# Kernel optimization log

Hardware: AMD Instinct MI355X
Metric: run time of the kernel (lower is better)

The kernel has to match this reference:

```python
import jax, jax.numpy as jnp
import numpy as np

VOCAB, EMBED, HIDDEN, FEAT = 193, 256, 512, 512
MAX_LEN = 15


def setup_inputs() -> dict:
    key = jax.random.key(0)
    ks = jax.random.split(key, 12)
    B = 8192
    s = 0.05  # small init scale for weights
    return {
        "img_feats": jax.random.normal(ks[0], (B, FEAT), jnp.float32),
        "text": jax.random.randint(ks[1], (B, MAX_LEN), 0, VOCAB, jnp.int64),
        "emb": jax.random.uniform(ks[2], (VOCAB, EMBED), jnp.float32, -0.1, 0.1),
        "W_proj": jax.random.normal(ks[3], (HIDDEN, FEAT), jnp.float32) * s,
        "b_proj": jnp.zeros((HIDDEN,), jnp.float32),
        "W_ih": jax.random.normal(ks[4], (3 * HIDDEN, EMBED), jnp.float32) * s,
        "W_hh": jax.random.normal(ks[5], (3 * HIDDEN, HIDDEN), jnp.float32) * s,
        "b_ih": jax.random.normal(ks[6], (3 * HIDDEN,), jnp.float32) * s,
        "b_hh": jax.random.normal(ks[7], (3 * HIDDEN,), jnp.float32) * s,
        "W_out": jax.random.uniform(ks[8], (VOCAB, HIDDEN), jnp.float32, -0.1, 0.1),
        "b_out": jnp.zeros((VOCAB,), jnp.float32),
    }


def reference(img_feats, text, emb, W_proj, b_proj, W_ih, W_hh, b_ih, b_hh, W_out, b_out):
    # h0 = project(img_feats)   [B, H]
    h0 = img_feats @ W_proj.T + b_proj
    # Teacher-forced decoder inputs: tokens text[:, 0..13] -> embeddings [T=14, B, E]
    xs = emb[text[:, : MAX_LEN - 1]].transpose(1, 0, 2)

    def gru_step(h, x):
        gi = x @ W_ih.T + b_ih   # [B, 3H]
        gh = h @ W_hh.T + b_hh   # [B, 3H]
        i_r, i_z, i_n = jnp.split(gi, 3, axis=-1)
        h_r, h_z, h_n = jnp.split(gh, 3, axis=-1)
        r = jax.nn.sigmoid(i_r + h_r)
        z = jax.nn.sigmoid(i_z + h_z)
        n = jnp.tanh(i_n + r * h_n)
        h_new = (1.0 - z) * n + z * h
        return h_new, h_new

    _, hs = jax.lax.scan(gru_step, h0, xs)  # hs: [T, B, H]
    preds = hs @ W_out.T + b_out            # [T, B, V]
    return preds.transpose(1, 0, 2)         # [B, T=14, V]
```

## Files before the change

kernel.cpp:

```cpp
#include <hip/hip_runtime.h>
#include <stdint.h>

using bf16x8 = __attribute__((ext_vector_type(8))) __bf16;
using f32x4  = __attribute__((ext_vector_type(4))) float;

#define AS1 __attribute__((address_space(1)))
#define AS3 __attribute__((address_space(3)))

constexpr size_t OFF_WHH   = 0;
constexpr size_t OFF_WPROJ = OFF_WHH   + (size_t)1536*512*2;
constexpr size_t OFF_WOUT  = OFF_WPROJ + (size_t)512*512*2;
constexpr size_t OFF_BHN   = OFF_WOUT  + (size_t)256*512*2;
constexpr size_t OFF_BPROJ = OFF_BHN   + 512*4;
constexpr size_t OFF_BOUT  = OFF_BPROJ + 512*4;
constexpr size_t OFF_EP    = OFF_BOUT  + 256*4;
constexpr size_t OFF_HS    = OFF_EP    + (size_t)193*1536*4;
constexpr size_t OFF_IMG   = OFF_HS    + (size_t)15*8192*512*2;
constexpr size_t WS_NEED   = OFF_IMG   + (size_t)8192*512*2;

__device__ __forceinline__ short f2bf(float f) {
  union { float f; unsigned u; } v; v.f = f;
  unsigned u = v.u;
  u += 0x7FFFu + ((u >> 16) & 1u);
  return (short)(u >> 16);
}
__device__ __forceinline__ float bf2f(short s) {
  union { float f; unsigned u; } v; v.u = ((unsigned)(unsigned short)s) << 16;
  return v.f;
}
__device__ __forceinline__ float sigm(float x) { return 1.f / (1.f + __expf(-x)); }
__device__ __forceinline__ float tanh_fast(float x) {
  x = fminf(fmaxf(x, -15.f), 15.f);
  float e = __expf(-2.f * x);
  return (1.f - e) / (1.f + e);
}

template<int ROWS, int WAVES>
__device__ __forceinline__ void stage_tile(const short* __restrict__ src, size_t row0,
                                           int stride, int k0, char* lds, int tid) {
  const int w = tid >> 6;
  const int lane = tid & 63;
#pragma unroll
  for (int s = 0; s < ROWS / (8 * WAVES); ++s) {
    const int rowbase = s * (8 * WAVES) + w * 8;
    const int row = rowbase + (lane >> 3);
    const int colE = ((lane & 7) ^ (row & 7)) * 8;
    const short* g = src + (row0 + (size_t)row) * (size_t)stride + k0 + colE;
    __builtin_amdgcn_global_load_lds((const AS1 int*)g, (AS3 int*)(lds + rowbase * 128),
                                     16, 0, 0);
  }
}

__device__ __forceinline__ bf16x8 read_frag(const char* lds, int row, int ks, int lane) {
  const int kb = ks * 64 + ((lane >> 4) << 4);
  return *(const bf16x8*)(lds + row * 128 + (kb ^ ((row & 7) << 4)));
}

__global__ void prep_kernel(const float* __restrict__ W_proj, const float* __restrict__ b_proj,
                            const float* __restrict__ W_hh, const float* __restrict__ b_hh,
                            const float* __restrict__ W_out, const float* __restrict__ b_out,
                            short* __restrict__ whh, short* __restrict__ wproj,
                            short* __restrict__ wout,
                            float* __restrict__ bhn, float* __restrict__ bproj,
                            float* __restrict__ bout) {
  const int total = 1536*512 + 512*512 + 256*512 + 512 + 512 + 256;
  const int stride = gridDim.x * blockDim.x;
  for (int i = blockIdx.x * blockDim.x + threadIdx.x; i < total; i += stride) {
    int j = i;
    if (j < 1536*512) { whh[j] = f2bf(W_hh[j]); continue; }
    j -= 1536*512;
    if (j < 512*512) { wproj[j] = f2bf(W_proj[j]); continue; }
    j -= 512*512;
    if (j < 256*512) {
      int r = j / 512, c = j % 512;
      wout[j] = f2bf(r < 193 ? W_out[r*512 + c] : 0.f);
      continue;
    }
    j -= 256*512;
    if (j < 512) { bhn[j] = b_hh[1024 + j]; continue; }
    j -= 512;
    if (j < 512) { bproj[j] = b_proj[j]; continue; }
    j -= 512;
    bout[j] = (j < 193) ? b_out[j] : 0.f;
  }
}

__global__ void embproj_kernel(const float* __restrict__ emb, const float* __restrict__ W_ih,
                               const float* __restrict__ b_ih, const float* __restrict__ b_hh,
                               float* __restrict__ ep) {
  const int idx = blockIdx.x * blockDim.x + threadIdx.x;
  if (idx >= 193 * 1536) return;
  const int v = idx / 1536, c = idx % 1536;
  const float* er = emb + (size_t)v * 256;
  const float* wr = W_ih + (size_t)c * 256;
  float s = 0.f;
#pragma unroll 4
  for (int k = 0; k < 256; k += 4) {
    const float4 a = *(const float4*)(er + k);
    const float4 b = *(const float4*)(wr + k);
    s += a.x * b.x + a.y * b.y + a.z * b.z + a.w * b.w;
  }
  s += b_ih[c] + (c < 1024 ? b_hh[c] : 0.f);
  ep[idx] = s;
}

__global__ void imgcvt_kernel(const float* __restrict__ img, short* __restrict__ imgbf) {
  const int i = blockIdx.x * blockDim.x + threadIdx.x;
  const float4 v = *(const float4*)(img + (size_t)i * 4);
  short4 o; o.x = f2bf(v.x); o.y = f2bf(v.y); o.z = f2bf(v.z); o.w = f2bf(v.w);
  *(short4*)(imgbf + (size_t)i * 4) = o;
}

template<int MODE>
__global__ __launch_bounds__(512, 1)
void gemm_kernel(const short* __restrict__ A, const short* __restrict__ Bw,
                 const float* __restrict__ bias, float* __restrict__ out_f,
                 short* __restrict__ out_bf) {
  __shared__ __align__(16) char smem[49152];
  char* ldsA = smem;
  char* ldsB = smem + 16384;
  const int tid = threadIdx.x;
  const int lane = tid & 63;
  const int w = tid >> 6;
  const int wr = w >> 2, wc = w & 3;
  const unsigned m0 = blockIdx.x * 128;
  const int j0 = blockIdx.y * 256;

  f32x4 acc[4][4];
#pragma unroll
  for (int a = 0; a < 4; ++a)
#pragma unroll
    for (int b = 0; b < 4; ++b) acc[a][b] = f32x4{0.f, 0.f, 0.f, 0.f};

  for (int it = 0; it < 8; ++it) {
    const int k0 = it * 64;
    __syncthreads();
    if (MODE == 0) {
      stage_tile<128, 8>(A, m0, 512, k0, ldsA, tid);
    } else {
#pragma unroll
      for (int s = 0; s < 2; ++s) {
        const int rowbase = s * 64 + w * 8;
        const int row = rowbase + (lane >> 3);
        const unsigned m = m0 + row;
        const unsigned b = m / 14u, t = m - b * 14u;
        const int colE = ((lane & 7) ^ (row & 7)) * 8;
        const short* g = A + ((size_t)t * 8192 + b) * 512 + k0 + colE;
        __builtin_amdgcn_global_load_lds((const AS1 int*)g, (AS3 int*)(ldsA + rowbase * 128),
                                         16, 0, 0);
      }
    }
    stage_tile<256, 8>(Bw, (size_t)j0, 512, k0, ldsB, tid);
    __syncthreads();
#pragma unroll
    for (int ks = 0; ks < 2; ++ks) {
      bf16x8 af[4];
#pragma unroll
      for (int mi = 0; mi < 4; ++mi)
        af[mi] = read_frag(ldsA, wr*64 + mi*16 + (lane & 15), ks, lane);
#pragma unroll
      for (int ji = 0; ji < 4; ++ji) {
        bf16x8 bfm = read_frag(ldsB, wc*64 + ji*16 + (lane & 15), ks, lane);
#pragma unroll
        for (int mi = 0; mi < 4; ++mi)
          acc[mi][ji] = __builtin_amdgcn_mfma_f32_16x16x32_bf16(af[mi], bfm, acc[mi][ji], 0, 0, 0);
      }
    }
  }
#pragma unroll
  for (int ji = 0; ji < 4; ++ji) {
    const int j = j0 + wc*64 + ji*16 + (lane & 15);
    const float bj = bias[j];
#pragma unroll
    for (int mi = 0; mi < 4; ++mi) {
#pragma unroll
      for (int i = 0; i < 4; ++i) {
        const size_t m = m0 + wr*64 + mi*16 + ((lane >> 4) * 4) + i;
        const float v = acc[mi][ji][i] + bj;
        if (MODE == 0) {
          out_bf[m * 512 + j] = f2bf(v);
        } else {
          if (j < 193) out_f[m * 193 + j] = v;
        }
      }
    }
  }
}

__global__ __launch_bounds__(256, 2)
void gate_kernel(const short* __restrict__ Hbf, const short* __restrict__ whh,
                 const int* __restrict__ text, const int t,
                 const float* __restrict__ embproj, const float* __restrict__ bhn,
                 short* __restrict__ hs_out) {
  __shared__ __align__(16) char smem[40960];
  char* ldsA = smem;
  char* ldsB = smem + 16384;
  const int tid = threadIdx.x;
  const int lane = tid & 63;
  const int w = tid >> 6;
  const int wr = w >> 1, wc = w & 1;
  const size_t m0 = (size_t)blockIdx.x * 128;
  const int j0 = blockIdx.y * 64;

  f32x4 acc_r[4][2], acc_z[4][2], acc_hn[4][2];
#pragma unroll
  for (int a = 0; a < 4; ++a)
#pragma unroll
    for (int b = 0; b < 2; ++b) {
      acc_r[a][b] = f32x4{0.f, 0.f, 0.f, 0.f};
      acc_z[a][b] = f32x4{0.f, 0.f, 0.f, 0.f};
      acc_hn[a][b] = f32x4{0.f, 0.f, 0.f, 0.f};
    }

  for (int it = 0; it < 8; ++it) {
    const int k0 = it * 64;
    __syncthreads();
    stage_tile<128, 4>(Hbf, m0, 512, k0, ldsA, tid);
#pragma unroll
    for (int g = 0; g < 3; ++g)
      stage_tile<64, 4>(whh, (size_t)(g * 512 + j0), 512, k0, ldsB + g * 8192, tid);
    __syncthreads();
#pragma unroll
    for (int ks = 0; ks < 2; ++ks) {
      bf16x8 af[4];
#pragma unroll
      for (int mi = 0; mi < 4; ++mi)
        af[mi] = read_frag(ldsA, wr*64 + mi*16 + (lane & 15), ks, lane);
#pragma unroll
      for (int ji = 0; ji < 2; ++ji) {
        const int nb = wc*32 + ji*16 + (lane & 15);
        bf16x8 b_r = read_frag(ldsB,         nb, ks, lane);
        bf16x8 b_z = read_frag(ldsB + 8192,  nb, ks, lane);
        bf16x8 b_n = read_frag(ldsB + 16384, nb, ks, lane);
#pragma unroll
        for (int mi = 0; mi < 4; ++mi) {
          acc_r[mi][ji]  = __builtin_amdgcn_mfma_f32_16x16x32_bf16(af[mi], b_r, acc_r[mi][ji], 0, 0, 0);
          acc_z[mi][ji]  = __builtin_amdgcn_mfma_f32_16x16x32_bf16(af[mi], b_z, acc_z[mi][ji], 0, 0, 0);
          acc_hn[mi][ji] = __builtin_amdgcn_mfma_f32_16x16x32_bf16(af[mi], b_n, acc_hn[mi][ji], 0, 0, 0);
        }
      }
    }
  }
  int toks[4][4];
#pragma unroll
  for (int mi = 0; mi < 4; ++mi)
#pragma unroll
    for (int i = 0; i < 4; ++i) {
      const size_t m = m0 + wr*64 + mi*16 + ((lane >> 4) * 4) + i;
      toks[mi][i] = text[m * 15 + t];
    }
#pragma unroll
  for (int ji = 0; ji < 2; ++ji) {
    const int j = j0 + wc*32 + ji*16 + (lane & 15);
    const float vbhn = bhn[j];
#pragma unroll
    for (int mi = 0; mi < 4; ++mi) {
#pragma unroll
      for (int i = 0; i < 4; ++i) {
        const size_t m = m0 + wr*64 + mi*16 + ((lane >> 4) * 4) + i;
        const float* ep = embproj + (size_t)toks[mi][i] * 1536;
        const float r = sigm(acc_r[mi][ji][i] + ep[j]);
        const float z = sigm(acc_z[mi][ji][i] + ep[512 + j]);
        const float n = tanh_fast(ep[1024 + j] + r * (acc_hn[mi][ji][i] + vbhn));
        const float hold = bf2f(Hbf[m * 512 + j]);
        hs_out[m * 512 + j] = f2bf((1.f - z) * n + z * hold);
      }
    }
  }
}

extern "C" void kernel_launch(void* const* d_in, const int* in_sizes, int n_in,
                              void* d_out, int out_size, void* d_ws, size_t ws_size,
                              hipStream_t stream) {
  (void)in_sizes; (void)n_in; (void)out_size;
  if (ws_size < WS_NEED) return;

  const float* img    = (const float*)d_in[0];
  const int*   text   = (const int*)  d_in[1];
  const float* emb    = (const float*)d_in[2];
  const float* W_proj = (const float*)d_in[3];
  const float* b_proj = (const float*)d_in[4];
  const float* W_ih   = (const float*)d_in[5];
  const float* W_hh   = (const float*)d_in[6];
  const float* b_ih   = (const float*)d_in[7];
  const float* b_hh   = (const float*)d_in[8];
  const float* W_out  = (const float*)d_in[9];
  const float* b_out  = (const float*)d_in[10];
  float* out = (float*)d_out;
  char* ws = (char*)d_ws;

  short* whh   = (short*)(ws + OFF_WHH);
  short* wproj = (short*)(ws + OFF_WPROJ);
  short* wout  = (short*)(ws + OFF_WOUT);
  float* bhn   = (float*)(ws + OFF_BHN);
  float* bproj = (float*)(ws + OFF_BPROJ);
  float* bout  = (float*)(ws + OFF_BOUT);
  float* ep    = (float*)(ws + OFF_EP);
  short* hs    = (short*)(ws + OFF_HS);
  short* imgbf = (short*)(ws + OFF_IMG);

  prep_kernel<<<512, 256, 0, stream>>>(W_proj, b_proj, W_hh, b_hh, W_out, b_out,
                                       whh, wproj, wout, bhn, bproj, bout);
  imgcvt_kernel<<<4096, 256, 0, stream>>>(img, imgbf);
  embproj_kernel<<<(193*1536 + 255)/256, 256, 0, stream>>>(emb, W_ih, b_ih, b_hh, ep);

  gemm_kernel<0><<<dim3(64, 2), 512, 0, stream>>>(imgbf, wproj, bproj, nullptr, hs);

  for (int t = 0; t < 14; ++t) {
    const short* Hb = hs + (size_t)t * 8192 * 512;
    short* Ho       = hs + (size_t)(t + 1) * 8192 * 512;
    gate_kernel<<<dim3(64, 8), 256, 0, stream>>>(Hb, whh, text, t, ep, bhn, Ho);
  }

  gemm_kernel<1><<<dim3(896, 1), 512, 0, stream>>>(hs + (size_t)8192 * 512, wout, bout,
                                                   out, nullptr);
}
```

Before: 419.2 us.

## Fuse GRU time loop into persistent kernel with grid barrier

Result: slower. 1.626 ms (+287.8%).

```diff
diff --git a/kernel.cpp b/kernel.cpp
--- a/kernel.cpp
+++ b/kernel.cpp
@@ -11,12 +11,15 @@
 constexpr size_t OFF_WPROJ = OFF_WHH   + (size_t)1536*512*2;
 constexpr size_t OFF_WOUT  = OFF_WPROJ + (size_t)512*512*2;
 constexpr size_t OFF_BHN   = OFF_WOUT  + (size_t)256*512*2;
-constexpr size_t OFF_BPROJ = OFF_BHN   + 512*4;
-constexpr size_t OFF_BOUT  = OFF_BPROJ + 512*4;
-constexpr size_t OFF_EP    = OFF_BOUT  + 256*4;
-constexpr size_t OFF_HS    = OFF_EP    + (size_t)193*1536*4;
+constexpr size_t OFF_BPROJ = OFF_BHN   + 2048;
+constexpr size_t OFF_BOUT  = OFF_BPROJ + 2048;
+constexpr size_t OFF_BAR   = OFF_BOUT  + 1024;
+constexpr size_t OFF_EP    = OFF_BAR   + 256;
+constexpr size_t OFF_HS    = OFF_EP    + (size_t)193*512*16;
 constexpr size_t OFF_IMG   = OFF_HS    + (size_t)15*8192*512*2;
 constexpr size_t WS_NEED   = OFF_IMG   + (size_t)8192*512*2;
+
+constexpr size_t SLAB = (size_t)8192 * 512;
 
 __device__ __forceinline__ short f2bf(float f) {
   union { float f; unsigned u; } v; v.f = f;
@@ -33,6 +36,18 @@
   x = fminf(fmaxf(x, -15.f), 15.f);
   float e = __expf(-2.f * x);
   return (1.f - e) / (1.f + e);
+}
+
+__device__ __forceinline__ void grid_barrier(unsigned* bar, unsigned target) {
+  __syncthreads();
+  if (threadIdx.x == 0) {
+    __threadfence();
+    __hip_atomic_fetch_add(bar, 1u, __ATOMIC_RELEASE, __HIP_MEMORY_SCOPE_AGENT);
+    while (__hip_atomic_load(bar, __ATOMIC_ACQUIRE, __HIP_MEMORY_SCOPE_AGENT) < target)
+      __builtin_amdgcn_s_sleep(8);
+    __threadfence();
+  }
+  __syncthreads();
 }
 
 template<int ROWS, int WAVES>
@@ -87,21 +102,29 @@
 
 __global__ void embproj_kernel(const float* __restrict__ emb, const float* __restrict__ W_ih,
                                const float* __restrict__ b_ih, const float* __restrict__ b_hh,
-                               float* __restrict__ ep) {
+                               float4* __restrict__ ep4) {
   const int idx = blockIdx.x * blockDim.x + threadIdx.x;
-  if (idx >= 193 * 1536) return;
-  const int v = idx / 1536, c = idx % 1536;
-  const float* er = emb + (size_t)v * 256;
-  const float* wr = W_ih + (size_t)c * 256;
-  float s = 0.f;
+  if (idx >= 193 * 512) return;
+  const int v = idx >> 9, j = idx & 511;
+  const float* er  = emb + (size_t)v * 256;
+  const float* w_r = W_ih + (size_t)j * 256;
+  const float* w_z = W_ih + (size_t)(512 + j) * 256;
+  const float* w_n = W_ih + (size_t)(1024 + j) * 256;
+  float sr = 0.f, sz = 0.f, sn = 0.f;
 #pragma unroll 4
   for (int k = 0; k < 256; k += 4) {
     const float4 a = *(const float4*)(er + k);
-    const float4 b = *(const float4*)(wr + k);
-    s += a.x * b.x + a.y * b.y + a.z * b.z + a.w * b.w;
-  }
-  s += b_ih[c] + (c < 1024 ? b_hh[c] : 0.f);
-  ep[idx] = s;
+    const float4 br = *(const float4*)(w_r + k);
+    const float4 bz = *(const float4*)(w_z + k);
+    const float4 bn = *(const float4*)(w_n + k);
+    sr += a.x*br.x + a.y*br.y + a.z*br.z + a.w*br.w;
+    sz += a.x*bz.x + a.y*bz.y + a.z*bz.z + a.w*bz.w;
+    sn += a.x*bn.x + a.y*bn.y + a.z*bn.z + a.w*bn.w;
+  }
+  sr += b_ih[j] + b_hh[j];
+  sz += b_ih[512 + j] + b_hh[512 + j];
+  sn += b_ih[1024 + j];
+  ep4[idx] = make_float4(sr, sz, sn, 0.f);
 }
 
 __global__ void imgcvt_kernel(const float* __restrict__ img, short* __restrict__ imgbf) {
@@ -188,10 +211,9 @@
 }
 
 __global__ __launch_bounds__(256, 2)
-void gate_kernel(const short* __restrict__ Hbf, const short* __restrict__ whh,
-                 const int* __restrict__ text, const int t,
-                 const float* __restrict__ embproj, const float* __restrict__ bhn,
-                 short* __restrict__ hs_out) {
+void gate_all_kernel(short* __restrict__ hs, const short* __restrict__ whh,
+                     const int* __restrict__ text, const float4* __restrict__ ep4,
+                     const float* __restrict__ bhn, unsigned* __restrict__ bar) {
   __shared__ __align__(16) char smem[40960];
   char* ldsA = smem;
   char* ldsB = smem + 16384;
@@ -201,71 +223,88 @@
   const int wr = w >> 1, wc = w & 1;
   const size_t m0 = (size_t)blockIdx.x * 128;
   const int j0 = blockIdx.y * 64;
-
-  f32x4 acc_r[4][2], acc_z[4][2], acc_hn[4][2];
-#pragma unroll
-  for (int a = 0; a < 4; ++a)
-#pragma unroll
-    for (int b = 0; b < 2; ++b) {
-      acc_r[a][b] = f32x4{0.f, 0.f, 0.f, 0.f};
-      acc_z[a][b] = f32x4{0.f, 0.f, 0.f, 0.f};
-      acc_hn[a][b] = f32x4{0.f, 0.f, 0.f, 0.f};
-    }
-
-  for (int it = 0; it < 8; ++it) {
-    const int k0 = it * 64;
-    __syncthreads();
-    stage_tile<128, 4>(Hbf, m0, 512, k0, ldsA, tid);
-#pragma unroll
-    for (int g = 0; g < 3; ++g)
-      stage_tile<64, 4>(whh, (size_t)(g * 512 + j0), 512, k0, ldsB + g * 8192, tid);
-    __syncthreads();
-#pragma unroll
-    for (int ks = 0; ks < 2; ++ks) {
-      bf16x8 af[4];
-#pragma unroll
-      for (int mi = 0; mi < 4; ++mi)
-        af[mi] = read_frag(ldsA, wr*64 + mi*16 + (lane & 15), ks, lane);
-#pragma unroll
-      for (int ji = 0; ji < 2; ++ji) {
-        const int nb = wc*32 + ji*16 + (lane & 15);
-        bf16x8 b_r = read_frag(ldsB,         nb, ks, lane);
-        bf16x8 b_z = read_frag(ldsB + 8192,  nb, ks, lane);
-        bf16x8 b_n = read_frag(ldsB + 16384, nb, ks, lane);
-#pragma unroll
-        for (int mi = 0; mi < 4; ++mi) {
-          acc_r[mi][ji]  = __builtin_amdgcn_mfma_f32_16x16x32_bf16(af[mi], b_r, acc_r[mi][ji], 0, 0, 0);
-          acc_z[mi][ji]  = __builtin_amdgcn_mfma_f32_16x16x32_bf16(af[mi], b_z, acc_z[mi][ji], 0, 0, 0);
-          acc_hn[mi][ji] = __builtin_amdgcn_mfma_f32_16x16x32_bf16(af[mi], b_n, acc_hn[mi][ji], 0, 0, 0);
-        }
-      }
-    }
-  }
-  int toks[4][4];
+  const unsigned nblocks = gridDim.x * gridDim.y;
+
+  int jj[2]; float vbhn[2];
+#pragma unroll
+  for (int ji = 0; ji < 2; ++ji) {
+    jj[ji] = j0 + wc*32 + ji*16 + (lane & 15);
+    vbhn[ji] = bhn[jj[ji]];
+  }
+  float hreg[4][4][2];
 #pragma unroll
   for (int mi = 0; mi < 4; ++mi)
 #pragma unroll
     for (int i = 0; i < 4; ++i) {
       const size_t m = m0 + wr*64 + mi*16 + ((lane >> 4) * 4) + i;
-      toks[mi][i] = text[m * 15 + t];
-    }
-#pragma unroll
-  for (int ji = 0; ji < 2; ++ji) {
-    const int j = j0 + wc*32 + ji*16 + (lane & 15);
-    const float vbhn = bhn[j];
+#pragma unroll
+      for (int ji = 0; ji < 2; ++ji)
+        hreg[mi][i][ji] = bf2f(hs[m * 512 + jj[ji]]);
+    }
+
+  for (int t = 0; t < 14; ++t) {
+    const short* Hbf = hs + (size_t)t * SLAB;
+    short* Ho       = hs + (size_t)(t + 1) * SLAB;
+
+    f32x4 acc_r[4][2], acc_z[4][2], acc_hn[4][2];
+#pragma unroll
+    for (int a = 0; a < 4; ++a)
+#pragma unroll
+      for (int b = 0; b < 2; ++b) {
+        acc_r[a][b] = f32x4{0.f, 0.f, 0.f, 0.f};
+        acc_z[a][b] = f32x4{0.f, 0.f, 0.f, 0.f};
+        acc_hn[a][b] = f32x4{0.f, 0.f, 0.f, 0.f};
+      }
+
+    for (int it = 0; it < 8; ++it) {
+      const int k0 = it * 64;
+      __syncthreads();
+      stage_tile<128, 4>(Hbf, m0, 512, k0, ldsA, tid);
+#pragma unroll
+      for (int g = 0; g < 3; ++g)
+        stage_tile<64, 4>(whh, (size_t)(g * 512 + j0), 512, k0, ldsB + g * 8192, tid);
+      __syncthreads();
+#pragma unroll
+      for (int ks = 0; ks < 2; ++ks) {
+        bf16x8 af[4];
+#pragma unroll
+        for (int mi = 0; mi < 4; ++mi)
+          af[mi] = read_frag(ldsA, wr*64 + mi*16 + (lane & 15), ks, lane);
+#pragma unroll
+        for (int ji = 0; ji < 2; ++ji) {
+          const int nb = wc*32 + ji*16 + (lane & 15);
+          bf16x8 b_r = read_frag(ldsB,         nb, ks, lane);
+          bf16x8 b_z = read_frag(ldsB + 8192,  nb, ks, lane);
+          bf16x8 b_n = read_frag(ldsB + 16384, nb, ks, lane);
+#pragma unroll
+          for (int mi = 0; mi < 4; ++mi) {
+            acc_r[mi][ji]  = __builtin_amdgcn_mfma_f32_16x16x32_bf16(af[mi], b_r, acc_r[mi][ji], 0, 0, 0);
+            acc_z[mi][ji]  = __builtin_amdgcn_mfma_f32_16x16x32_bf16(af[mi], b_z, acc_z[mi][ji], 0, 0, 0);
+            acc_hn[mi][ji] = __builtin_amdgcn_mfma_f32_16x16x32_bf16(af[mi], b_n, acc_hn[mi][ji], 0, 0, 0);
+          }
+        }
+      }
+    }
 #pragma unroll
     for (int mi = 0; mi < 4; ++mi) {
 #pragma unroll
       for (int i = 0; i < 4; ++i) {
         const size_t m = m0 + wr*64 + mi*16 + ((lane >> 4) * 4) + i;
-        const float* ep = embproj + (size_t)toks[mi][i] * 1536;
-        const float r = sigm(acc_r[mi][ji][i] + ep[j]);
-        const float z = sigm(acc_z[mi][ji][i] + ep[512 + j]);
-        const float n = tanh_fast(ep[1024 + j] + r * (acc_hn[mi][ji][i] + vbhn));
-        const float hold = bf2f(Hbf[m * 512 + j]);
-        hs_out[m * 512 + j] = f2bf((1.f - z) * n + z * hold);
-      }
-    }
+        const int tok = text[m * 15 + t];
+#pragma unroll
+        for (int ji = 0; ji < 2; ++ji) {
+          const float4 e = ep4[(size_t)tok * 512 + jj[ji]];
+          const float r = sigm(acc_r[mi][ji][i] + e.x);
+          const float z = sigm(acc_z[mi][ji][i] + e.y);
+          const float n = tanh_fast(e.z + r * (acc_hn[mi][ji][i] + vbhn[ji]));
+          const float hv = (1.f - z) * n + z * hreg[mi][i][ji];
+          const short hb = f2bf(hv);
+          Ho[m * 512 + jj[ji]] = hb;
+          hreg[mi][i][ji] = bf2f(hb);
+        }
+      }
+    }
+    if (t < 13) grid_barrier(bar, nblocks * (unsigned)(t + 1));
   }
 }
 
@@ -295,22 +334,20 @@
   float* bhn   = (float*)(ws + OFF_BHN);
   float* bproj = (float*)(ws + OFF_BPROJ);
   float* bout  = (float*)(ws + OFF_BOUT);
-  float* ep    = (float*)(ws + OFF_EP);
+  unsigned* bar = (unsigned*)(ws + OFF_BAR);
+  float4* ep4  = (float4*)(ws + OFF_EP);
   short* hs    = (short*)(ws + OFF_HS);
   short* imgbf = (short*)(ws + OFF_IMG);
 
+  hipMemsetAsync(bar, 0, 256, stream);
   prep_kernel<<<512, 256, 0, stream>>>(W_proj, b_proj, W_hh, b_hh, W_out, b_out,
                                        whh, wproj, wout, bhn, bproj, bout);
   imgcvt_kernel<<<4096, 256, 0, stream>>>(img, imgbf);
-  embproj_kernel<<<(193*1536 + 255)/256, 256, 0, stream>>>(emb, W_ih, b_ih, b_hh, ep);
+  embproj_kernel<<<(193*512 + 255)/256, 256, 0, stream>>>(emb, W_ih, b_ih, b_hh, ep4);
 
   gemm_kernel<0><<<dim3(64, 2), 512, 0, stream>>>(imgbf, wproj, bproj, nullptr, hs);
 
-  for (int t = 0; t < 14; ++t) {
-    const short* Hb = hs + (size_t)t * 8192 * 512;
-    short* Ho       = hs + (size_t)(t + 1) * 8192 * 512;
-    gate_kernel<<<dim3(64, 8), 256, 0, stream>>>(Hb, whh, text, t, ep, bhn, Ho);
-  }
+  gate_all_kernel<<<dim3(64, 8), 256, 0, stream>>>(hs, whh, text, ep4, bhn, bar);
 
   gemm_kernel<1><<<dim3(896, 1), 512, 0, stream>>>(hs + (size_t)8192 * 512, wout, bout,
                                                    out, nullptr);
```
